# Kernel optimization log

Measured on AMD Instinct MI355X. Metric: run time of the kernel, lower is better.

Reference implementation:

```python
import math
import jax, jax.numpy as jnp
import numpy as np

H, C, PQ, PV = 8, 256, 8, 12   # no_heads, c_hidden, no_qk_points, no_v_points
INF, EPS = 1e5, 1e-8

def quat_to_rot(q):
    w, x, y, z = q[..., 0], q[..., 1], q[..., 2], q[..., 3]
    r = jnp.stack([
        1 - 2*(y*y + z*z), 2*(x*y - w*z),     2*(x*z + w*y),
        2*(x*y + w*z),     1 - 2*(x*x + z*z), 2*(y*z - w*x),
        2*(x*z - w*y),     2*(y*z + w*x),     1 - 2*(x*x + y*y),
    ], axis=-1)
    return r.reshape(q.shape[:-1] + (3, 3))

def setup_inputs() -> dict:
    key = jax.random.key(0)
    ks = jax.random.split(key, 16)
    B, N, CS, CZ = 1, 512, 384, 128
    s = jax.random.normal(ks[0], (B, N, CS), jnp.float32)
    z = jax.random.normal(ks[1], (B, N, N, CZ), jnp.float32) * 0.1
    quat = jax.random.normal(ks[2], (B, N, 4), jnp.float32)
    quat = quat / jnp.linalg.norm(quat, axis=-1, keepdims=True)
    rot = quat_to_rot(quat)                       # [B,N,3,3] valid rotations
    trans = jax.random.normal(ks[3], (B, N, 3), jnp.float32) * 10.0
    mask = jnp.ones((B, N), jnp.float32)
    g = lambda k, sh: jax.random.normal(k, sh, jnp.float32) * 0.02
    params = dict(
        wq=g(ks[4], (CS, H*C)), bq=jnp.zeros((H*C,), jnp.float32),
        wkv=g(ks[5], (CS, 2*H*C)), bkv=jnp.zeros((2*H*C,), jnp.float32),
        wqp=g(ks[6], (CS, H*PQ*3)), bqp=jnp.zeros((H*PQ*3,), jnp.float32),
        wkvp=g(ks[7], (CS, H*(PQ+PV)*3)), bkvp=jnp.zeros((H*(PQ+PV)*3,), jnp.float32),
        wb=g(ks[8], (CZ, H)), bb=jnp.zeros((H,), jnp.float32),
        wz=g(ks[9], (CZ, CZ//4)), bz=jnp.zeros((CZ//4,), jnp.float32),
        head_weights=jnp.full((H,), 0.541324854612918, jnp.float32),  # softplus^-1(1)
        wo=g(ks[10], (H*(C + 4*PV + CZ//4), CS)), bo=jnp.zeros((CS,), jnp.float32),
    )
    return dict(s=s, z=z, rot=rot, trans=trans, mask=mask, **params)

def reference(s, z, rot, trans, mask, wq, bq, wkv, bkv, wqp, bqp, wkvp, bkvp, wb, bb, wz, bz, head_weights, wo, bo):
    B, N, CS = s.shape
    q = (s @ wq + bq).reshape(B, N, H, C)
    kv = (s @ wkv + bkv).reshape(B, N, H, 2 * C)
    k, v = kv[..., :C], kv[..., C:]

    def split_pts(x):  # torch split-into-3 + stack(-1): [B,N,3*M] -> [B,N,M,3]
        return jnp.moveaxis(x.reshape(B, N, 3, -1), -2, -1)

    def apply_rigid(p):  # global frame: R @ p + t
        return jnp.einsum('bnij,bnpj->bnpi', rot, p) + trans[:, :, None, :]

    q_pts = apply_rigid(split_pts(s @ wqp + bqp)).reshape(B, N, H, PQ, 3)
    kv_pts = apply_rigid(split_pts(s @ wkvp + bkvp)).reshape(B, N, H, PQ + PV, 3)
    k_pts, v_pts = kv_pts[..., :PQ, :], kv_pts[..., PQ:, :]

    b_bias = z @ wb + bb                                  # [B,Ni,Nj,H]
    a = jnp.einsum('bihc,bjhc->bhij', q, k) * math.sqrt(1.0 / (3 * C))
    a = a + math.sqrt(1.0 / 3) * jnp.moveaxis(b_bias, -1, 1)

    disp = q_pts[:, :, None] - k_pts[:, None]             # [B,Ni,Nj,H,PQ,3]
    pt_att = jnp.sum(disp * disp, axis=-1)                # [B,Ni,Nj,H,PQ]
    hw = jax.nn.softplus(head_weights) * math.sqrt(1.0 / (3 * (PQ * 9.0 / 2)))
    pt_att = -0.5 * jnp.sum(pt_att * hw[None, None, None, :, None], axis=-1)  # [B,Ni,Nj,H]

    sq_mask = INF * (mask[:, :, None] * mask[:, None, :] - 1.0)
    a = a + jnp.moveaxis(pt_att, -1, 1) + sq_mask[:, None]
    a = jax.nn.softmax(a, axis=-1)                        # [B,H,Ni,Nj]

    o = jnp.einsum('bhij,bjhc->bihc', a, v).reshape(B, N, H * C)

    o_pt = jnp.einsum('bhij,bjhpd->bihpd', a, v_pts)      # [B,N,H,PV,3] global
    o_pt = jnp.einsum('bnji,bnhpj->bnhpi', rot, o_pt - trans[:, :, None, None, :])  # invert_apply
    o_pt_norm = jnp.sqrt(jnp.sum(o_pt * o_pt, axis=-1) + EPS).reshape(B, N, H * PV)
    o_pt_flat = o_pt.reshape(B, N, H * PV, 3)

    pair_z = z @ wz + bz                                  # [B,Ni,Nj,CZ//4]
    o_pair = jnp.einsum('bhij,bijd->bihd', a, pair_z).reshape(B, N, -1)

    feats = jnp.concatenate(
        [o, o_pt_flat[..., 0], o_pt_flat[..., 1], o_pt_flat[..., 2], o_pt_norm, o_pair], axis=-1)
    return feats @ wo + bo
```

## Files before the change

### kernel.cpp

```cpp
#include <hip/hip_runtime.h>


#define OFF_QBH    0
#define OFF_KBH    524288
#define OFF_VB     1048576
#define OFF_QPRAW  2097152
#define OFF_KVPRAW 2195456
#define OFF_QPTS   2441216
#define OFF_KVPTS  2539520
#define OFF_BBIAS  2785280
#define OFF_PAIRZT 3833856
#define OFF_ATTNH  8028160
#define OFF_ATTNL  9076736
#define OFF_FEATS  10125312
#define OFF_WCAT   11501568
#define OFF_WTALL  11504640
#define OFF_VPT    12819456

typedef __attribute__((ext_vector_type(8))) short short8;
typedef __attribute__((ext_vector_type(4))) float f32x4;

__device__ __forceinline__ unsigned short f2bf(float f) {
  union { float f; unsigned u; } v; v.f = f;
  unsigned u = v.u;
  unsigned r = (u + 0x7fffu + ((u >> 16) & 1u)) >> 16;
  return (unsigned short)r;
}
__device__ __forceinline__ float bf2f(unsigned short h) {
  union { unsigned u; float f; } v; v.u = ((unsigned)h) << 16; return v.f;
}
__device__ __forceinline__ short8 pack8(float4 a, float4 b) {
  short8 r;
  r[0] = (short)f2bf(a.x); r[1] = (short)f2bf(a.y);
  r[2] = (short)f2bf(a.z); r[3] = (short)f2bf(a.w);
  r[4] = (short)f2bf(b.x); r[5] = (short)f2bf(b.y);
  r[6] = (short)f2bf(b.z); r[7] = (short)f2bf(b.w);
  return r;
}

__device__ __forceinline__ void sgemm_tile64(
    const float* __restrict__ A, const float* __restrict__ W,
    const float* bias, float* __restrict__ Cout,
    const int K, const int Ncol, const int row0, const int col0,
    const int k0b, const int k1, const bool atomic,
    float (*As)[64], float (*Bs)[64]) {
  const int t  = threadIdx.x;
  const int tx = t & 15, ty = t >> 4;
  const int am = t >> 2, akq = (t & 3) << 2;
  const int bk = t >> 4, bn = (t & 15) << 2;
  float acc[4][4];
#pragma unroll
  for (int i = 0; i < 4; i++)
#pragma unroll
    for (int j = 0; j < 4; j++) acc[i][j] = 0.f;

  for (int k0 = k0b; k0 < k1; k0 += 16) {
    float4 a4 = *(const float4*)(A + (size_t)(row0 + am) * K + k0 + akq);
    float4 b4 = *(const float4*)(W + (size_t)(k0 + bk) * Ncol + col0 + bn);
    __syncthreads();
    As[akq + 0][am] = a4.x; As[akq + 1][am] = a4.y;
    As[akq + 2][am] = a4.z; As[akq + 3][am] = a4.w;
    *(float4*)&Bs[bk][bn] = b4;
    __syncthreads();
#pragma unroll
    for (int kk = 0; kk < 16; kk++) {
      float4 av = *(const float4*)&As[kk][ty << 2];
      float4 bv = *(const float4*)&Bs[kk][tx << 2];
      acc[0][0] += av.x * bv.x; acc[0][1] += av.x * bv.y; acc[0][2] += av.x * bv.z; acc[0][3] += av.x * bv.w;
      acc[1][0] += av.y * bv.x; acc[1][1] += av.y * bv.y; acc[1][2] += av.y * bv.z; acc[1][3] += av.y * bv.w;
      acc[2][0] += av.z * bv.x; acc[2][1] += av.z * bv.y; acc[2][2] += av.z * bv.z; acc[2][3] += av.z * bv.w;
      acc[3][0] += av.w * bv.x; acc[3][1] += av.w * bv.y; acc[3][2] += av.w * bv.z; acc[3][3] += av.w * bv.w;
    }
  }
#pragma unroll
  for (int i = 0; i < 4; i++) {
    int row = row0 + (ty << 2) + i;
#pragma unroll
    for (int j = 0; j < 4; j++) {
      int col = col0 + (tx << 2) + j;
      float v = acc[i][j] + (bias ? bias[col] : 0.f);
      if (atomic) atomicAdd(&Cout[(size_t)row * Ncol + col], v);
      else Cout[(size_t)row * Ncol + col] = v;
    }
  }
}

__global__ __launch_bounds__(256) void prep_wT_all(
    const float* __restrict__ wq, const float* __restrict__ wkv,
    const float* __restrict__ wqp, const float* __restrict__ wkvp,
    unsigned short* __restrict__ wTall) {
  const int ntile = blockIdx.x, kt = blockIdx.y;
  const float* src; int Nsrc, nloc0;
  const int ng0 = ntile * 64;
  if (ntile < 32)      { src = wq;   Nsrc = 2048; nloc0 = ng0; }
  else if (ntile < 96) { src = wkv;  Nsrc = 4096; nloc0 = ng0 - 2048; }
  else if (ntile < 99) { src = wqp;  Nsrc = 192;  nloc0 = ng0 - 6144; }
  else                 { src = wkvp; Nsrc = 480;  nloc0 = ng0 - 6336; }
  __shared__ float tile[64][65];
  const int t = threadIdx.x;
  const int r = t >> 2, cs = (t & 3) * 16;
#pragma unroll
  for (int i = 0; i < 16; i += 4) {
    int n = nloc0 + cs + i;
    float4 v;
    if (n + 3 < Nsrc) v = *(const float4*)(src + (size_t)(kt * 64 + r) * Nsrc + n);
    else {
      v.x = (n + 0 < Nsrc) ? src[(size_t)(kt * 64 + r) * Nsrc + n + 0] : 0.f;
      v.y = (n + 1 < Nsrc) ? src[(size_t)(kt * 64 + r) * Nsrc + n + 1] : 0.f;
      v.z = (n + 2 < Nsrc) ? src[(size_t)(kt * 64 + r) * Nsrc + n + 2] : 0.f;
      v.w = (n + 3 < Nsrc) ? src[(size_t)(kt * 64 + r) * Nsrc + n + 3] : 0.f;
    }
    tile[r][cs + i + 0] = v.x; tile[r][cs + i + 1] = v.y;
    tile[r][cs + i + 2] = v.z; tile[r][cs + i + 3] = v.w;
  }
  __syncthreads();
  const int nr = t >> 2, ks = (t & 3) * 16;
  unsigned short ov[16];
#pragma unroll
  for (int i = 0; i < 16; i++) ov[i] = f2bf(tile[ks + i][nr]);
  unsigned short* dst = wTall + (size_t)(ng0 + nr) * 384 + kt * 64 + ks;
  *(uint4*)(dst) = *(const uint4*)&ov[0];
  *(uint4*)(dst + 8) = *(const uint4*)&ov[8];
}

__global__ __launch_bounds__(256) void proj_mfma(
    const float* __restrict__ s, const unsigned short* __restrict__ wTall,
    const float* __restrict__ bq, const float* __restrict__ bkv,
    const float* __restrict__ bqp, const float* __restrict__ bkvp,
    unsigned short* __restrict__ qbh, unsigned short* __restrict__ kbh,
    float* __restrict__ vb, float* __restrict__ qpraw, float* __restrict__ kvpraw) {
  const int bx = blockIdx.x, row0 = blockIdx.y * 64;
  const int lane = threadIdx.x & 63, wv = threadIdx.x >> 6;
  const int quad = lane >> 4, m = lane & 15;
  const int n0 = bx * 64;
  const float* srow = s + (size_t)(row0 + wv * 16 + m) * 384;
  f32x4 acc[4];
#pragma unroll
  for (int nt = 0; nt < 4; nt++) acc[nt] = (f32x4){0.f, 0.f, 0.f, 0.f};

#pragma unroll
  for (int ksx = 0; ksx < 12; ksx++) {
    const int c0 = ksx * 32 + quad * 8;
    float4 a0 = *(const float4*)(srow + c0);
    float4 a1 = *(const float4*)(srow + c0 + 4);
    short8 af = pack8(a0, a1);
#pragma unroll
    for (int nt = 0; nt < 4; nt++) {
      short8 bf = *(const short8*)(wTall + (size_t)(n0 + nt * 16 + m) * 384 + c0);
      acc[nt] = __builtin_amdgcn_mfma_f32_16x16x32_bf16(af, bf, acc[nt], 0, 0, 0);
    }
  }

  const int rbase = row0 + wv * 16 + quad * 4;
#pragma unroll
  for (int nt = 0; nt < 4; nt++) {
    const int col = n0 + nt * 16 + m;
    if (n0 < 2048) {
      const float bias = bq[col];
#pragma unroll
      for (int r = 0; r < 4; r++)
        qbh[(size_t)(rbase + r) * 2048 + col] = f2bf(acc[nt][r] + bias);
    } else if (n0 < 6144) {
      const int ckv = col - 2048;
      const float bias = bkv[ckv];
      const int hh = ckv >> 9, c = ckv & 511;
      if (c < 256) {
#pragma unroll
        for (int r = 0; r < 4; r++)
          kbh[(size_t)(rbase + r) * 2048 + hh * 256 + c] = f2bf(acc[nt][r] + bias);
      } else {
#pragma unroll
        for (int r = 0; r < 4; r++)
          vb[(size_t)(rbase + r) * 2048 + hh * 256 + (c - 256)] = acc[nt][r] + bias;
      }
    } else if (n0 < 6336) {
      const int cq = col - 6144;
      const float bias = bqp[cq];
#pragma unroll
      for (int r = 0; r < 4; r++)
        qpraw[(size_t)(rbase + r) * 192 + cq] = acc[nt][r] + bias;
    } else {
      const int ck = col - 6336;
      if (ck < 480) {
        const float bias = bkvp[ck];
#pragma unroll
        for (int r = 0; r < 4; r++)
          kvpraw[(size_t)(rbase + r) * 480 + ck] = acc[nt][r] + bias;
      }
    }
  }
}

__global__ __launch_bounds__(256) void rigid_pts(
    const float* __restrict__ qpraw, const float* __restrict__ kvpraw,
    const float* __restrict__ rot, const float* __restrict__ trans,
    float* __restrict__ qpts, float* __restrict__ kvpts) {
  int gid = blockIdx.x * 256 + threadIdx.x;
  int n = gid / 224, r = gid % 224;
  const float* R  = rot + n * 9;
  const float* tr = trans + n * 3;
  float px, py, pz; float* dst;
  if (r < 64) {
    const float* src = qpraw + (size_t)n * 192;
    px = src[r]; py = src[64 + r]; pz = src[128 + r];
    dst = qpts + ((size_t)n * 64 + r) * 3;
  } else {
    int p = r - 64;
    const float* src = kvpraw + (size_t)n * 480;
    px = src[p]; py = src[160 + p]; pz = src[320 + p];
    dst = kvpts + ((size_t)n * 160 + p) * 3;
  }
  dst[0] = R[0] * px + R[1] * py + R[2] * pz + tr[0];
  dst[1] = R[3] * px + R[4] * py + R[5] * pz + tr[1];
  dst[2] = R[6] * px + R[7] * py + R[8] * pz + tr[2];
}

__global__ __launch_bounds__(256) void prep_wT(
    const float* __restrict__ wb, const float* __restrict__ wz,
    unsigned short* __restrict__ wT) {
  int l = blockIdx.x * 256 + threadIdx.x;
  if (l < 6144) {
    int n = l >> 7, k = l & 127;
    float v = (n < 8) ? wb[k * 8 + n] * 0.5773502691896258f
                      : (n < 40 ? wz[k * 32 + (n - 8)] : 0.f);
    wT[l] = f2bf(v);
  }
}

__global__ __launch_bounds__(256) void zpass_mfma(
    const float* __restrict__ z, const unsigned short* __restrict__ wT,
    const float* __restrict__ bb, const float* __restrict__ bz,
    unsigned short* __restrict__ bbias_tb, unsigned short* __restrict__ pairzT) {
  __shared__ __align__(16) unsigned short lb[4][8][16];
  __shared__ __align__(16) unsigned short lp[4][32][16];
  const int lane = threadIdx.x & 63;
  const int wave = threadIdx.x >> 6;
  const int quad = lane >> 4, m = lane & 15;
  const int tile = blockIdx.x * 4 + wave;
  const int row0 = tile * 16;

  short8 bf[3][4];
#pragma unroll
  for (int nt = 0; nt < 3; nt++)
#pragma unroll
    for (int s = 0; s < 4; s++)
      bf[nt][s] = *(const short8*)(wT + (size_t)(nt * 16 + m) * 128 + s * 32 + quad * 8);

  float bias[3];
#pragma unroll
  for (int nt = 0; nt < 3; nt++) {
    int c = nt * 16 + m;
    bias[nt] = (c < 8) ? 0.5773502691896258f * bb[c] : (c < 40 ? bz[c - 8] : 0.f);
  }

  f32x4 acc[3];
#pragma unroll
  for (int nt = 0; nt < 3; nt++) acc[nt] = (f32x4){0.f, 0.f, 0.f, 0.f};

  const float* zr = z + (size_t)(row0 + m) * 128 + quad * 8;
#pragma unroll
  for (int s = 0; s < 4; s++) {
    float4 a0 = *(const float4*)(zr + s * 32);
    float4 a1 = *(const float4*)(zr + s * 32 + 4);
    short8 af = pack8(a0, a1);
#pragma unroll
    for (int nt = 0; nt < 3; nt++)
      acc[nt] = __builtin_amdgcn_mfma_f32_16x16x32_bf16(af, bf[nt][s], acc[nt], 0, 0, 0);
  }

#pragma unroll
  for (int nt = 0; nt < 3; nt++) {
    const int c = nt * 16 + m;
#pragma unroll
    for (int r = 0; r < 4; r++) {
      const float v = acc[nt][r] + bias[nt];
      const int jl = quad * 4 + r;
      if (c < 8)       lb[wave][c][jl] = f2bf(v);
      else if (c < 40) lp[wave][c - 8][jl] = f2bf(v);
    }
  }
  const int i = row0 >> 9, j0 = row0 & 511;
  if (lane < 16) {
    int c = lane >> 1, half = lane & 1;
    uint4 val = *(const uint4*)&lb[wave][c][half * 8];
    *(uint4*)(bbias_tb + (size_t)c * 262144 + row0 + half * 8) = val;
  }
  {
    int d = lane >> 1, half = lane & 1;
    uint4 val = *(const uint4*)&lp[wave][d][half * 8];
    *(uint4*)(pairzT + ((size_t)i * 32 + d) * 512 + j0 + half * 8) = val;
  }
}

__global__ __launch_bounds__(256) void vpt_prep(
    const float* __restrict__ vb, const float* __restrict__ kvpts,
    unsigned short* __restrict__ vptT) {
  const int jt = blockIdx.x, h = blockIdx.y, part = blockIdx.z;
  const int j0 = jt * 64, t = threadIdx.x;
  if (part < 4) {
    __shared__ float tile[64][65];
    const int c0 = part * 64;
    const int r = t >> 2, cs = (t & 3) * 16;
#pragma unroll
    for (int ii = 0; ii < 16; ii += 4) {
      float4 v = *(const float4*)(vb + (size_t)(j0 + r) * 2048 + h * 256 + c0 + cs + ii);
      tile[r][cs + ii + 0] = v.x; tile[r][cs + ii + 1] = v.y;
      tile[r][cs + ii + 2] = v.z; tile[r][cs + ii + 3] = v.w;
    }
    __syncthreads();
    const int cl = t >> 2, js = (t & 3) * 16;
    unsigned short ov[16];
#pragma unroll
    for (int x = 0; x < 16; x++) ov[x] = f2bf(tile[js + x][cl]);
    unsigned short* dst = vptT + ((size_t)h * 352 + c0 + cl) * 512 + j0 + js;
    *(uint4*)dst = *(const uint4*)&ov[0];
    *(uint4*)(dst + 8) = *(const uint4*)&ov[8];
  } else {
    __shared__ float lds[64][37];
    for (int l = t; l < 64 * 36; l += 256) {
      int jl = l / 36, w = l % 36;
      lds[jl][w] = kvpts[((size_t)(j0 + jl) * 160 + h * 20 + 8) * 3 + w];
    }
    __syncthreads();
#pragma unroll
    for (int step = 0; step < 3; step++) {
      int chunk = t + 256 * step;
      int row = chunk >> 3, js = (chunk & 7) * 8;
      unsigned short ov[8];
#pragma unroll
      for (int x = 0; x < 8; x++) {
        int w = (row < 48) ? row : row - 48;
        float f = (w < 36) ? lds[js + x][w] : 0.f;
        unsigned short hi = f2bf(f);
        ov[x] = (row < 48) ? hi : f2bf(f - bf2f(hi));
      }
      *(uint4*)(vptT + ((size_t)h * 352 + 256 + row) * 512 + j0 + js) = *(const uint4*)&ov[0];
    }
  }
}

__global__ __launch_bounds__(256) void logits_softmax(
    const unsigned short* __restrict__ qbh, const unsigned short* __restrict__ kbh,
    const float* __restrict__ qpts, const float* __restrict__ kvpts,
    const unsigned short* __restrict__ bbias_tb, const float* __restrict__ mask,
    const float* __restrict__ hwp,
    unsigned short* __restrict__ attnh, unsigned short* __restrict__ attnl) {
  const int it = blockIdx.x, h = blockIdx.y;
  const int i0 = it * 16;
  __shared__ __align__(16) unsigned short kph[512][32], kpl[512][32];
  __shared__ __align__(16) unsigned short qph[16][32], qpl[16][32];
  __shared__ float kp2[512], qp2[16];
  __shared__ float redm[16][4], reds[16][4];
  __shared__ __align__(16) unsigned short sth[4][16][128], stl[4][16][128];
  const int t = threadIdx.x;

#pragma unroll
  for (int rr = 0; rr < 2; rr++) {
    const int j = t * 2 + rr;
    const float* src = kvpts + ((size_t)j * 160 + h * 20) * 3;
    float s2 = 0.f;
#pragma unroll
    for (int w = 0; w < 24; w++) {
      float x = src[w];
      unsigned short hi = f2bf(x);
      kph[j][w] = hi; kpl[j][w] = f2bf(x - bf2f(hi));
      s2 += x * x;
    }
#pragma unroll
    for (int w = 24; w < 32; w++) { kph[j][w] = 0; kpl[j][w] = 0; }
    kp2[j] = s2;
  }
  if (t < 16) {
    const float* src = qpts + ((size_t)(i0 + t) * 64 + h * 8) * 3;
    float s2 = 0.f;
#pragma unroll
    for (int w = 0; w < 24; w++) {
      float x = src[w];
      unsigned short hi = f2bf(x);
      qph[t][w] = hi; qpl[t][w] = f2bf(x - bf2f(hi));
      s2 += x * x;
    }
#pragma unroll
    for (int w = 24; w < 32; w++) { qph[t][w] = 0; qpl[t][w] = 0; }
    qp2[t] = s2;
  }
  __syncthreads();

  const int lane = t & 63, wv = t >> 6;
  const int quad = lane >> 4, m = lane & 15;
  const int jw0 = wv * 128;

  f32x4 acc[8];
#pragma unroll
  for (int nt = 0; nt < 8; nt++) acc[nt] = (f32x4){0.f, 0.f, 0.f, 0.f};
  const unsigned short* qrow = qbh + (size_t)(i0 + m) * 2048 + h * 256;
#pragma unroll
  for (int s = 0; s < 8; s++) {
    short8 af = *(const short8*)(qrow + s * 32 + quad * 8);
#pragma unroll
    for (int nt = 0; nt < 8; nt++) {
      short8 bfr = *(const short8*)(kbh + (size_t)(jw0 + nt * 16 + m) * 2048 + h * 256 + s * 32 + quad * 8);
      acc[nt] = __builtin_amdgcn_mfma_f32_16x16x32_bf16(af, bfr, acc[nt], 0, 0, 0);
    }
  }

  short8 aqh = *(const short8*)&qph[m][quad * 8];
  short8 aql = *(const short8*)&qpl[m][quad * 8];
  f32x4 accp[8];
#pragma unroll
  for (int nt = 0; nt < 8; nt++) {
    short8 bkh = *(const short8*)&kph[jw0 + nt * 16 + m][quad * 8];
    short8 bkl = *(const short8*)&kpl[jw0 + nt * 16 + m][quad * 8];
    f32x4 p = (f32x4){0.f, 0.f, 0.f, 0.f};
    p = __builtin_amdgcn_mfma_f32_16x16x32_bf16(aqh, bkh, p, 0, 0, 0);
    p = __builtin_amdgcn_mfma_f32_16x16x32_bf16(aqh, bkl, p, 0, 0, 0);
    p = __builtin_amdgcn_mfma_f32_16x16x32_bf16(aql, bkh, p, 0, 0, 0);
    accp[nt] = p;
  }

  const float c1 = 0.03608439182435161f;
  const float hw = log1pf(expf(hwp[h])) * 0.09622504486493764f;
  float lg[8][4];
  float rmax[4] = {-1e30f, -1e30f, -1e30f, -1e30f};
#pragma unroll
  for (int nt = 0; nt < 8; nt++) {
    const int j = jw0 + nt * 16 + m;
    const float kp2v = kp2[j];
    const float mj = mask[j];
#pragma unroll
    for (int r = 0; r < 4; r++) {
      const int il = quad * 4 + r;
      const float pt = qp2[il] + kp2v - 2.f * accp[nt][r];
      float v = c1 * acc[nt][r]
              + bf2f(bbias_tb[(size_t)h * 262144 + (size_t)(i0 + il) * 512 + j])
              - 0.5f * hw * pt
              + 100000.f * (mask[i0 + il] * mj - 1.f);
      lg[nt][r] = v;
      rmax[r] = fmaxf(rmax[r], v);
    }
  }
#pragma unroll
  for (int r = 0; r < 4; r++) {
#pragma unroll
    for (int off = 1; off < 16; off <<= 1) rmax[r] = fmaxf(rmax[r], __shfl_xor(rmax[r], off));
  }
  if (m == 0) {
#pragma unroll
    for (int r = 0; r < 4; r++) redm[quad * 4 + r][wv] = rmax[r];
  }
  __syncthreads();
  float rowm[4], rsum[4];
#pragma unroll
  for (int r = 0; r < 4; r++) {
    const int il = quad * 4 + r;
    rowm[r] = fmaxf(fmaxf(redm[il][0], redm[il][1]), fmaxf(redm[il][2], redm[il][3]));
    rsum[r] = 0.f;
  }
#pragma unroll
  for (int nt = 0; nt < 8; nt++)
#pragma unroll
    for (int r = 0; r < 4; r++) {
      float e = __expf(lg[nt][r] - rowm[r]);
      lg[nt][r] = e;
      rsum[r] += e;
    }
#pragma unroll
  for (int r = 0; r < 4; r++) {
#pragma unroll
    for (int off = 1; off < 16; off <<= 1) rsum[r] += __shfl_xor(rsum[r], off);
  }
  if (m == 0) {
#pragma unroll
    for (int r = 0; r < 4; r++) reds[quad * 4 + r][wv] = rsum[r];
  }
  __syncthreads();
  float inv[4];
#pragma unroll
  for (int r = 0; r < 4; r++) {
    const int il = quad * 4 + r;
    inv[r] = 1.f / (reds[il][0] + reds[il][1] + reds[il][2] + reds[il][3]);
  }
#pragma unroll
  for (int nt = 0; nt < 8; nt++)
#pragma unroll
    for (int r = 0; r < 4; r++) {
      const int il = quad * 4 + r;
      float a = lg[nt][r] * inv[r];
      unsigned short hi = f2bf(a);
      sth[wv][il][nt * 16 + m] = hi;
      stl[wv][il][nt * 16 + m] = f2bf(a - bf2f(hi));
    }
#pragma unroll
  for (int step = 0; step < 4; step++) {
    const int idx = lane + 64 * step;
    const int il = idx >> 4, seg = idx & 15;
    uint4 vh = *(const uint4*)&sth[wv][il][seg * 8];
    uint4 vl = *(const uint4*)&stl[wv][il][seg * 8];
    const size_t off = ((size_t)h * 512 + i0 + il) * 512 + jw0 + seg * 8;
    *(uint4*)(attnh + off) = vh;
    *(uint4*)(attnl + off) = vl;
  }
}

__global__ __launch_bounds__(256) void attn_v3(
    const unsigned short* __restrict__ attnh, const unsigned short* __restrict__ attnl,
    const unsigned short* __restrict__ vptT,
    const float* __restrict__ rot, const float* __restrict__ trans,
    float* __restrict__ feats) {
  const int it = blockIdx.x, h = blockIdx.y;
  const int i0 = it * 16;
  __shared__ float lds_h[16][48], lds_l[16][48];
  const int t = threadIdx.x;
  const int lane = t & 63, wv = t >> 6;
  const int quad = lane >> 4, m = lane & 15;
  const int nt0 = wv * 6;
  const int ncnt = (wv == 3) ? 4 : 6;

  f32x4 acc[6];
#pragma unroll
  for (int k = 0; k < 6; k++) acc[k] = (f32x4){0.f, 0.f, 0.f, 0.f};

  const size_t arow = ((size_t)h * 512 + i0 + m) * 512;
  const unsigned short* vbase = vptT + (size_t)h * 352 * 512;
#pragma unroll
  for (int s = 0; s < 16; s++) {
    const int ko = s * 32 + quad * 8;
    short8 ah = *(const short8*)(attnh + arow + ko);
    short8 al = *(const short8*)(attnl + arow + ko);
#pragma unroll
    for (int k = 0; k < 6; k++) {
      if (k < ncnt) {
        const int nt = nt0 + k;
        short8 bfr = *(const short8*)(vbase + (size_t)(nt * 16 + m) * 512 + ko);
        acc[k] = __builtin_amdgcn_mfma_f32_16x16x32_bf16(ah, bfr, acc[k], 0, 0, 0);
        if (nt >= 16 && nt < 19)
          acc[k] = __builtin_amdgcn_mfma_f32_16x16x32_bf16(al, bfr, acc[k], 0, 0, 0);
      }
    }
  }

#pragma unroll
  for (int k = 0; k < 6; k++) {
    if (k < ncnt) {
      const int nt = nt0 + k;
      if (nt < 16) {
#pragma unroll
        for (int r = 0; r < 4; r++)
          feats[(size_t)(i0 + quad * 4 + r) * 2688 + h * 256 + nt * 16 + m] = acc[k][r];
      } else if (nt < 19) {
        const int w = (nt - 16) * 16 + m;
#pragma unroll
        for (int r = 0; r < 4; r++) if (w < 36) lds_h[quad * 4 + r][w] = acc[k][r];
      } else {
        const int w = (nt - 19) * 16 + m;
#pragma unroll
        for (int r = 0; r < 4; r++) if (w < 36) lds_l[quad * 4 + r][w] = acc[k][r];
      }
    }
  }
  __syncthreads();
  if (t < 192) {
    const int il = t / 12, p = t % 12, irow = i0 + il;
    const float* R = rot + irow * 9;
    const float* tr = trans + irow * 3;
    float x  = lds_h[il][p * 3 + 0] + lds_l[il][p * 3 + 0] - tr[0];
    float y  = lds_h[il][p * 3 + 1] + lds_l[il][p * 3 + 1] - tr[1];
    float zz = lds_h[il][p * 3 + 2] + lds_l[il][p * 3 + 2] - tr[2];
    float o0 = R[0] * x + R[3] * y + R[6] * zz;
    float o1 = R[1] * x + R[4] * y + R[7] * zz;
    float o2 = R[2] * x + R[5] * y + R[8] * zz;
    float nrm = sqrtf(o0 * o0 + o1 * o1 + o2 * o2 + 1e-8f);
    float* fr = feats + (size_t)irow * 2688 + 2048;
    fr[h * 12 + p]       = o0;
    fr[96 + h * 12 + p]  = o1;
    fr[192 + h * 12 + p] = o2;
    fr[288 + h * 12 + p] = nrm;
  }
}

__global__ __launch_bounds__(256) void o_pair_mfma(
    const unsigned short* __restrict__ attnh, const unsigned short* __restrict__ pairzT,
    float* __restrict__ feats) {
  const int lane = threadIdx.x & 63, wv = threadIdx.x >> 6;
  const int quad = lane >> 4, m = lane & 15;
  const int i = blockIdx.x * 4 + wv;
  f32x4 acc[2];
  acc[0] = (f32x4){0.f, 0.f, 0.f, 0.f};
  acc[1] = (f32x4){0.f, 0.f, 0.f, 0.f};
#pragma unroll
  for (int s = 0; s < 16; s++) {
    const int ko = s * 32 + quad * 8;
    short8 af = *(const short8*)(attnh + (size_t)(m & 7) * 262144 + (size_t)i * 512 + ko);
#pragma unroll
    for (int nt = 0; nt < 2; nt++) {
      short8 bfr = *(const short8*)(pairzT + ((size_t)i * 32 + nt * 16 + m) * 512 + ko);
      acc[nt] = __builtin_amdgcn_mfma_f32_16x16x32_bf16(af, bfr, acc[nt], 0, 0, 0);
    }
  }
  if (quad < 2) {
#pragma unroll
    for (int nt = 0; nt < 2; nt++)
#pragma unroll
      for (int r = 0; r < 4; r++) {
        const int hh = quad * 4 + r, d = nt * 16 + m;
        feats[(size_t)i * 2688 + 2432 + hh * 32 + d] = acc[nt][r];
      }
  }
}

__global__ __launch_bounds__(256) void out_gemm_kernel(
    const float* __restrict__ feats, const float* __restrict__ wo,
    const float* __restrict__ bo, float* __restrict__ out) {
  __shared__ float As[16][64], Bs[16][64];
  int col0 = blockIdx.x * 64, row0 = blockIdx.y * 64;
  int k0 = blockIdx.z * 336;
  sgemm_tile64(feats, wo, blockIdx.z == 0 ? bo : nullptr, out,
               2688, 384, row0, col0, k0, k0 + 336, true, As, Bs);
}

extern "C" void kernel_launch(void* const* d_in, const int* in_sizes, int n_in,
                              void* d_out, int out_size, void* d_ws, size_t ws_size,
                              hipStream_t stream) {
  const float* s     = (const float*)d_in[0];
  const float* z     = (const float*)d_in[1];
  const float* rot   = (const float*)d_in[2];
  const float* trans = (const float*)d_in[3];
  const float* mask  = (const float*)d_in[4];
  const float* wq    = (const float*)d_in[5];
  const float* bq    = (const float*)d_in[6];
  const float* wkv   = (const float*)d_in[7];
  const float* bkv   = (const float*)d_in[8];
  const float* wqp   = (const float*)d_in[9];
  const float* bqp   = (const float*)d_in[10];
  const float* wkvp  = (const float*)d_in[11];
  const float* bkvp  = (const float*)d_in[12];
  const float* wb    = (const float*)d_in[13];
  const float* bb    = (const float*)d_in[14];
  const float* wz    = (const float*)d_in[15];
  const float* bz    = (const float*)d_in[16];
  const float* hwp   = (const float*)d_in[17];
  const float* wo    = (const float*)d_in[18];
  const float* bo    = (const float*)d_in[19];
  float* out = (float*)d_out;

  float* ws = (float*)d_ws;
  unsigned short* qbh   = (unsigned short*)(ws + OFF_QBH);
  unsigned short* kbh   = (unsigned short*)(ws + OFF_KBH);
  float* vb      = ws + OFF_VB;
  float* qpraw   = ws + OFF_QPRAW;
  float* kvpraw  = ws + OFF_KVPRAW;
  float* qpts    = ws + OFF_QPTS;
  float* kvpts   = ws + OFF_KVPTS;
  unsigned short* bbias_tb = (unsigned short*)(ws + OFF_BBIAS);
  unsigned short* pairzT   = (unsigned short*)(ws + OFF_PAIRZT);
  unsigned short* attnh    = (unsigned short*)(ws + OFF_ATTNH);
  unsigned short* attnl    = (unsigned short*)(ws + OFF_ATTNL);
  float* feats   = ws + OFF_FEATS;
  unsigned short* wT    = (unsigned short*)(ws + OFF_WCAT);
  unsigned short* wTall = (unsigned short*)(ws + OFF_WTALL);
  unsigned short* vptT  = (unsigned short*)(ws + OFF_VPT);

  prep_wT_all<<<dim3(107, 6), 256, 0, stream>>>(wq, wkv, wqp, wkvp, wTall);
  prep_wT<<<24, 256, 0, stream>>>(wb, wz, wT);
  proj_mfma<<<dim3(107, 8), 256, 0, stream>>>(s, wTall, bq, bkv, bqp, bkvp,
                                              qbh, kbh, vb, qpraw, kvpraw);
  rigid_pts<<<448, 256, 0, stream>>>(qpraw, kvpraw, rot, trans, qpts, kvpts);
  zpass_mfma<<<4096, 256, 0, stream>>>(z, wT, bb, bz, bbias_tb, pairzT);
  vpt_prep<<<dim3(8, 8, 5), 256, 0, stream>>>(vb, kvpts, vptT);
  logits_softmax<<<dim3(32, 8), 256, 0, stream>>>(qbh, kbh, qpts, kvpts, bbias_tb,
                                                  mask, hwp, attnh, attnl);
  attn_v3<<<dim3(32, 8), 256, 0, stream>>>(attnh, attnl, vptT, rot, trans, feats);
  o_pair_mfma<<<128, 256, 0, stream>>>(attnh, pairzT, feats);
  (void)hipMemsetAsync(out, 0, (size_t)out_size * sizeof(float), stream);
  out_gemm_kernel<<<dim3(6, 8, 8), 256, 0, stream>>>(feats, wo, bo, out);
}
```

Before: 390.2 us.

## Fuse softmax with attention-value MFMA, precompute point planes, use bf16 MFMA output GEMM

The attention-value product now runs inside the logits/softmax kernel, reading the softmax hi/lo tiles straight from shared memory instead of writing and re-reading attnl and attn through global memory. Query/key point hi/lo bf16 planes and squared norms are computed once by a new small kernel rather than redundantly per block. The fp32 SIMT split-K output GEMM with atomics and a memset is replaced by a bf16 MFMA GEMM over a bf16 features buffer and a pre-transposed bf16 wo. This trades fp32 precision in the final projection for cheaper compute and removes launches and atomics.

```diff
diff --git a/kernel.cpp b/kernel.cpp
--- a/kernel.cpp
+++ b/kernel.cpp
@@ -11,11 +11,17 @@
 #define OFF_BBIAS  2785280
 #define OFF_PAIRZT 3833856
 #define OFF_ATTNH  8028160
-#define OFF_ATTNL  9076736
-#define OFF_FEATS  10125312
-#define OFF_WCAT   11501568
-#define OFF_WTALL  11504640
-#define OFF_VPT    12819456
+#define OFF_FEATSB 9076736
+#define OFF_WCAT   9764864
+#define OFF_WTALL  9767936
+#define OFF_VPT    11082752
+#define OFF_WOT    11803648
+#define OFF_QPTH   12319744
+#define OFF_QPTL   12385280
+#define OFF_KPTH   12450816
+#define OFF_KPTL   12516352
+#define OFF_QP2    12581888
+#define OFF_KP2    12585984
 
 typedef __attribute__((ext_vector_type(8))) short short8;
 typedef __attribute__((ext_vector_type(4))) float f32x4;
@@ -36,53 +42,6 @@
   r[4] = (short)f2bf(b.x); r[5] = (short)f2bf(b.y);
   r[6] = (short)f2bf(b.z); r[7] = (short)f2bf(b.w);
   return r;
-}
-
-__device__ __forceinline__ void sgemm_tile64(
-    const float* __restrict__ A, const float* __restrict__ W,
-    const float* bias, float* __restrict__ Cout,
-    const int K, const int Ncol, const int row0, const int col0,
-    const int k0b, const int k1, const bool atomic,
-    float (*As)[64], float (*Bs)[64]) {
-  const int t  = threadIdx.x;
-  const int tx = t & 15, ty = t >> 4;
-  const int am = t >> 2, akq = (t & 3) << 2;
-  const int bk = t >> 4, bn = (t & 15) << 2;
-  float acc[4][4];
-#pragma unroll
-  for (int i = 0; i < 4; i++)
-#pragma unroll
-    for (int j = 0; j < 4; j++) acc[i][j] = 0.f;
-
-  for (int k0 = k0b; k0 < k1; k0 += 16) {
-    float4 a4 = *(const float4*)(A + (size_t)(row0 + am) * K + k0 + akq);
-    float4 b4 = *(const float4*)(W + (size_t)(k0 + bk) * Ncol + col0 + bn);
-    __syncthreads();
-    As[akq + 0][am] = a4.x; As[akq + 1][am] = a4.y;
-    As[akq + 2][am] = a4.z; As[akq + 3][am] = a4.w;
-    *(float4*)&Bs[bk][bn] = b4;
-    __syncthreads();
-#pragma unroll
-    for (int kk = 0; kk < 16; kk++) {
-      float4 av = *(const float4*)&As[kk][ty << 2];
-      float4 bv = *(const float4*)&Bs[kk][tx << 2];
-      acc[0][0] += av.x * bv.x; acc[0][1] += av.x * bv.y; acc[0][2] += av.x * bv.z; acc[0][3] += av.x * bv.w;
-      acc[1][0] += av.y * bv.x; acc[1][1] += av.y * bv.y; acc[1][2] += av.y * bv.z; acc[1][3] += av.y * bv.w;
-      acc[2][0] += av.z * bv.x; acc[2][1] += av.z * bv.y; acc[2][2] += av.z * bv.z; acc[2][3] += av.z * bv.w;
-      acc[3][0] += av.w * bv.x; acc[3][1] += av.w * bv.y; acc[3][2] += av.w * bv.z; acc[3][3] += av.w * bv.w;
-    }
-  }
-#pragma unroll
-  for (int i = 0; i < 4; i++) {
-    int row = row0 + (ty << 2) + i;
-#pragma unroll
-    for (int j = 0; j < 4; j++) {
-      int col = col0 + (tx << 2) + j;
-      float v = acc[i][j] + (bias ? bias[col] : 0.f);
-      if (atomic) atomicAdd(&Cout[(size_t)row * Ncol + col], v);
-      else Cout[(size_t)row * Ncol + col] = v;
-    }
-  }
 }
 
 __global__ __launch_bounds__(256) void prep_wT_all(
@@ -119,6 +78,28 @@
 #pragma unroll
   for (int i = 0; i < 16; i++) ov[i] = f2bf(tile[ks + i][nr]);
   unsigned short* dst = wTall + (size_t)(ng0 + nr) * 384 + kt * 64 + ks;
+  *(uint4*)(dst) = *(const uint4*)&ov[0];
+  *(uint4*)(dst + 8) = *(const uint4*)&ov[8];
+}
+
+__global__ __launch_bounds__(256) void prep_woT(
+    const float* __restrict__ wo, unsigned short* __restrict__ woT) {
+  const int kt = blockIdx.x, ntile = blockIdx.y;
+  __shared__ float tile[64][65];
+  const int t = threadIdx.x;
+  const int r = t >> 2, cs = (t & 3) * 16;
+#pragma unroll
+  for (int i = 0; i < 16; i += 4) {
+    float4 v = *(const float4*)(wo + (size_t)(kt * 64 + r) * 384 + ntile * 64 + cs + i);
+    tile[r][cs + i + 0] = v.x; tile[r][cs + i + 1] = v.y;
+    tile[r][cs + i + 2] = v.z; tile[r][cs + i + 3] = v.w;
+  }
+  __syncthreads();
+  const int nr = t >> 2, ks = (t & 3) * 16;
+  unsigned short ov[16];
+#pragma unroll
+  for (int i = 0; i < 16; i++) ov[i] = f2bf(tile[ks + i][nr]);
+  unsigned short* dst = woT + (size_t)(ntile * 64 + nr) * 2688 + kt * 64 + ks;
   *(uint4*)(dst) = *(const uint4*)&ov[0];
   *(uint4*)(dst + 8) = *(const uint4*)&ov[8];
 }
@@ -215,6 +196,55 @@
   dst[2] = R[6] * px + R[7] * py + R[8] * pz + tr[2];
 }
 
+__global__ __launch_bounds__(256) void pts_planes(
+    const float* __restrict__ qpts, const float* __restrict__ kvpts,
+    unsigned short* __restrict__ qptH, unsigned short* __restrict__ qptL,
+    unsigned short* __restrict__ kptH, unsigned short* __restrict__ kptL,
+    float* __restrict__ qp2g, float* __restrict__ kp2g) {
+  const int row = blockIdx.x * 256 + threadIdx.x;
+  const int h = blockIdx.y;
+  {
+    const float* src = qpts + ((size_t)row * 64 + h * 8) * 3;
+    unsigned short hi[32], lo[32]; float s2 = 0.f;
+#pragma unroll
+    for (int w = 0; w < 24; w++) {
+      float x = src[w];
+      hi[w] = f2bf(x); lo[w] = f2bf(x - bf2f(hi[w]));
+      s2 += x * x;
+    }
+#pragma unroll
+    for (int w = 24; w < 32; w++) { hi[w] = 0; lo[w] = 0; }
+    unsigned short* dh = qptH + ((size_t)h * 512 + row) * 32;
+    unsigned short* dl = qptL + ((size_t)h * 512 + row) * 32;
+#pragma unroll
+    for (int g = 0; g < 4; g++) {
+      *(uint4*)(dh + g * 8) = *(const uint4*)&hi[g * 8];
+      *(uint4*)(dl + g * 8) = *(const uint4*)&lo[g * 8];
+    }
+    qp2g[h * 512 + row] = s2;
+  }
+  {
+    const float* src = kvpts + ((size_t)row * 160 + h * 20) * 3;
+    unsigned short hi[32], lo[32]; float s2 = 0.f;
+#pragma unroll
+    for (int w = 0; w < 24; w++) {
+      float x = src[w];
+      hi[w] = f2bf(x); lo[w] = f2bf(x - bf2f(hi[w]));
+      s2 += x * x;
+    }
+#pragma unroll
+    for (int w = 24; w < 32; w++) { hi[w] = 0; lo[w] = 0; }
+    unsigned short* dh = kptH + ((size_t)h * 512 + row) * 32;
+    unsigned short* dl = kptL + ((size_t)h * 512 + row) * 32;
+#pragma unroll
+    for (int g = 0; g < 4; g++) {
+      *(uint4*)(dh + g * 8) = *(const uint4*)&hi[g * 8];
+      *(uint4*)(dl + g * 8) = *(const uint4*)&lo[g * 8];
+    }
+    kp2g[h * 512 + row] = s2;
+  }
+}
+
 __global__ __launch_bounds__(256) void prep_wT(
     const float* __restrict__ wb, const float* __restrict__ wz,
     unsigned short* __restrict__ wT) {
@@ -339,53 +369,21 @@
   }
 }
 
-__global__ __launch_bounds__(256) void logits_softmax(
+__global__ __launch_bounds__(256) void logits_fused(
     const unsigned short* __restrict__ qbh, const unsigned short* __restrict__ kbh,
-    const float* __restrict__ qpts, const float* __restrict__ kvpts,
+    const unsigned short* __restrict__ qptH, const unsigned short* __restrict__ qptL,
+    const unsigned short* __restrict__ kptH, const unsigned short* __restrict__ kptL,
+    const float* __restrict__ qp2g, const float* __restrict__ kp2g,
     const unsigned short* __restrict__ bbias_tb, const float* __restrict__ mask,
-    const float* __restrict__ hwp,
-    unsigned short* __restrict__ attnh, unsigned short* __restrict__ attnl) {
+    const float* __restrict__ hwp, const unsigned short* __restrict__ vptT,
+    const float* __restrict__ rot, const float* __restrict__ trans,
+    unsigned short* __restrict__ attnh, unsigned short* __restrict__ featsb) {
   const int it = blockIdx.x, h = blockIdx.y;
   const int i0 = it * 16;
-  __shared__ __align__(16) unsigned short kph[512][32], kpl[512][32];
-  __shared__ __align__(16) unsigned short qph[16][32], qpl[16][32];
-  __shared__ float kp2[512], qp2[16];
+  __shared__ __align__(16) unsigned short sth[4][16][136], stl[4][16][136];
   __shared__ float redm[16][4], reds[16][4];
-  __shared__ __align__(16) unsigned short sth[4][16][128], stl[4][16][128];
+  __shared__ float lds_h[16][48], lds_l[16][48];
   const int t = threadIdx.x;
-
-#pragma unroll
-  for (int rr = 0; rr < 2; rr++) {
-    const int j = t * 2 + rr;
-    const float* src = kvpts + ((size_t)j * 160 + h * 20) * 3;
-    float s2 = 0.f;
-#pragma unroll
-    for (int w = 0; w < 24; w++) {
-      float x = src[w];
-      unsigned short hi = f2bf(x);
-      kph[j][w] = hi; kpl[j][w] = f2bf(x - bf2f(hi));
-      s2 += x * x;
-    }
-#pragma unroll
-    for (int w = 24; w < 32; w++) { kph[j][w] = 0; kpl[j][w] = 0; }
-    kp2[j] = s2;
-  }
-  if (t < 16) {
-    const float* src = qpts + ((size_t)(i0 + t) * 64 + h * 8) * 3;
-    float s2 = 0.f;
-#pragma unroll
-    for (int w = 0; w < 24; w++) {
-      float x = src[w];
-      unsigned short hi = f2bf(x);
-      qph[t][w] = hi; qpl[t][w] = f2bf(x - bf2f(hi));
-      s2 += x * x;
-    }
-#pragma unroll
-    for (int w = 24; w < 32; w++) { qph[t][w] = 0; qpl[t][w] = 0; }
-    qp2[t] = s2;
-  }
-  __syncthreads();
-
   const int lane = t & 63, wv = t >> 6;
   const int quad = lane >> 4, m = lane & 15;
   const int jw0 = wv * 128;
@@ -404,13 +402,14 @@
     }
   }
 
-  short8 aqh = *(const short8*)&qph[m][quad * 8];
-  short8 aql = *(const short8*)&qpl[m][quad * 8];
+  short8 aqh = *(const short8*)(qptH + ((size_t)h * 512 + i0 + m) * 32 + quad * 8);
+  short8 aql = *(const short8*)(qptL + ((size_t)h * 512 + i0 + m) * 32 + quad * 8);
   f32x4 accp[8];
 #pragma unroll
   for (int nt = 0; nt < 8; nt++) {
-    short8 bkh = *(const short8*)&kph[jw0 + nt * 16 + m][quad * 8];
-    short8 bkl = *(const short8*)&kpl[jw0 + nt * 16 + m][quad * 8];
+    const size_t krow = ((size_t)h * 512 + jw0 + nt * 16 + m) * 32 + quad * 8;
+    short8 bkh = *(const short8*)(kptH + krow);
+    short8 bkl = *(const short8*)(kptL + krow);
     f32x4 p = (f32x4){0.f, 0.f, 0.f, 0.f};
     p = __builtin_amdgcn_mfma_f32_16x16x32_bf16(aqh, bkh, p, 0, 0, 0);
     p = __builtin_amdgcn_mfma_f32_16x16x32_bf16(aqh, bkl, p, 0, 0, 0);
@@ -420,17 +419,20 @@
 
   const float c1 = 0.03608439182435161f;
   const float hw = log1pf(expf(hwp[h])) * 0.09622504486493764f;
+  float qp2v[4];
+#pragma unroll
+  for (int r = 0; r < 4; r++) qp2v[r] = qp2g[h * 512 + i0 + quad * 4 + r];
   float lg[8][4];
   float rmax[4] = {-1e30f, -1e30f, -1e30f, -1e30f};
 #pragma unroll
   for (int nt = 0; nt < 8; nt++) {
     const int j = jw0 + nt * 16 + m;
-    const float kp2v = kp2[j];
+    const float kp2v = kp2g[h * 512 + j];
     const float mj = mask[j];
 #pragma unroll
     for (int r = 0; r < 4; r++) {
       const int il = quad * 4 + r;
-      const float pt = qp2[il] + kp2v - 2.f * accp[nt][r];
+      const float pt = qp2v[r] + kp2v - 2.f * accp[nt][r];
       float v = c1 * acc[nt][r]
               + bf2f(bbias_tb[(size_t)h * 262144 + (size_t)(i0 + il) * 512 + j])
               - 0.5f * hw * pt
@@ -490,55 +492,38 @@
       sth[wv][il][nt * 16 + m] = hi;
       stl[wv][il][nt * 16 + m] = f2bf(a - bf2f(hi));
     }
+  __syncthreads();
 #pragma unroll
   for (int step = 0; step < 4; step++) {
     const int idx = lane + 64 * step;
     const int il = idx >> 4, seg = idx & 15;
     uint4 vh = *(const uint4*)&sth[wv][il][seg * 8];
-    uint4 vl = *(const uint4*)&stl[wv][il][seg * 8];
-    const size_t off = ((size_t)h * 512 + i0 + il) * 512 + jw0 + seg * 8;
-    *(uint4*)(attnh + off) = vh;
-    *(uint4*)(attnl + off) = vl;
-  }
-}
-
-__global__ __launch_bounds__(256) void attn_v3(
-    const unsigned short* __restrict__ attnh, const unsigned short* __restrict__ attnl,
-    const unsigned short* __restrict__ vptT,
-    const float* __restrict__ rot, const float* __restrict__ trans,
-    float* __restrict__ feats) {
-  const int it = blockIdx.x, h = blockIdx.y;
-  const int i0 = it * 16;
-  __shared__ float lds_h[16][48], lds_l[16][48];
-  const int t = threadIdx.x;
-  const int lane = t & 63, wv = t >> 6;
-  const int quad = lane >> 4, m = lane & 15;
+    *(uint4*)(attnh + ((size_t)h * 512 + i0 + il) * 512 + jw0 + seg * 8) = vh;
+  }
+
   const int nt0 = wv * 6;
   const int ncnt = (wv == 3) ? 4 : 6;
-
-  f32x4 acc[6];
-#pragma unroll
-  for (int k = 0; k < 6; k++) acc[k] = (f32x4){0.f, 0.f, 0.f, 0.f};
-
-  const size_t arow = ((size_t)h * 512 + i0 + m) * 512;
+  f32x4 vacc[6];
+#pragma unroll
+  for (int k = 0; k < 6; k++) vacc[k] = (f32x4){0.f, 0.f, 0.f, 0.f};
   const unsigned short* vbase = vptT + (size_t)h * 352 * 512;
 #pragma unroll
   for (int s = 0; s < 16; s++) {
+    const int wsrc = s >> 2, col = (s & 3) * 32 + quad * 8;
+    short8 ah = *(const short8*)&sth[wsrc][m][col];
+    short8 al = *(const short8*)&stl[wsrc][m][col];
     const int ko = s * 32 + quad * 8;
-    short8 ah = *(const short8*)(attnh + arow + ko);
-    short8 al = *(const short8*)(attnl + arow + ko);
 #pragma unroll
     for (int k = 0; k < 6; k++) {
       if (k < ncnt) {
         const int nt = nt0 + k;
         short8 bfr = *(const short8*)(vbase + (size_t)(nt * 16 + m) * 512 + ko);
-        acc[k] = __builtin_amdgcn_mfma_f32_16x16x32_bf16(ah, bfr, acc[k], 0, 0, 0);
+        vacc[k] = __builtin_amdgcn_mfma_f32_16x16x32_bf16(ah, bfr, vacc[k], 0, 0, 0);
         if (nt >= 16 && nt < 19)
-          acc[k] = __builtin_amdgcn_mfma_f32_16x16x32_bf16(al, bfr, acc[k], 0, 0, 0);
+          vacc[k] = __builtin_amdgcn_mfma_f32_16x16x32_bf16(al, bfr, vacc[k], 0, 0, 0);
       }
     }
   }
-
 #pragma unroll
   for (int k = 0; k < 6; k++) {
     if (k < ncnt) {
@@ -546,15 +531,15 @@
       if (nt < 16) {
 #pragma unroll
         for (int r = 0; r < 4; r++)
-          feats[(size_t)(i0 + quad * 4 + r) * 2688 + h * 256 + nt * 16 + m] = acc[k][r];
+          featsb[(size_t)(i0 + quad * 4 + r) * 2688 + h * 256 + nt * 16 + m] = f2bf(vacc[k][r]);
       } else if (nt < 19) {
         const int w = (nt - 16) * 16 + m;
 #pragma unroll
-        for (int r = 0; r < 4; r++) if (w < 36) lds_h[quad * 4 + r][w] = acc[k][r];
+        for (int r = 0; r < 4; r++) if (w < 36) lds_h[quad * 4 + r][w] = vacc[k][r];
       } else {
         const int w = (nt - 19) * 16 + m;
 #pragma unroll
-        for (int r = 0; r < 4; r++) if (w < 36) lds_l[quad * 4 + r][w] = acc[k][r];
+        for (int r = 0; r < 4; r++) if (w < 36) lds_l[quad * 4 + r][w] = vacc[k][r];
       }
     }
   }
@@ -570,17 +555,17 @@
     float o1 = R[1] * x + R[4] * y + R[7] * zz;
     float o2 = R[2] * x + R[5] * y + R[8] * zz;
     float nrm = sqrtf(o0 * o0 + o1 * o1 + o2 * o2 + 1e-8f);
-    float* fr = feats + (size_t)irow * 2688 + 2048;
-    fr[h * 12 + p]       = o0;
-    fr[96 + h * 12 + p]  = o1;
-    fr[192 + h * 12 + p] = o2;
-    fr[288 + h * 12 + p] = nrm;
+    unsigned short* fr = featsb + (size_t)irow * 2688 + 2048;
+    fr[h * 12 + p]       = f2bf(o0);
+    fr[96 + h * 12 + p]  = f2bf(o1);
+    fr[192 + h * 12 + p] = f2bf(o2);
+    fr[288 + h * 12 + p] = f2bf(nrm);
   }
 }
 
 __global__ __launch_bounds__(256) void o_pair_mfma(
     const unsigned short* __restrict__ attnh, const unsigned short* __restrict__ pairzT,
-    float* __restrict__ feats) {
+    unsigned short* __restrict__ featsb) {
   const int lane = threadIdx.x & 63, wv = threadIdx.x >> 6;
   const int quad = lane >> 4, m = lane & 15;
   const int i = blockIdx.x * 4 + wv;
@@ -603,19 +588,32 @@
 #pragma unroll
       for (int r = 0; r < 4; r++) {
         const int hh = quad * 4 + r, d = nt * 16 + m;
-        feats[(size_t)i * 2688 + 2432 + hh * 32 + d] = acc[nt][r];
+        featsb[(size_t)i * 2688 + 2432 + hh * 32 + d] = f2bf(acc[nt][r]);
       }
   }
 }
 
-__global__ __launch_bounds__(256) void out_gemm_kernel(
-    const float* __restrict__ feats, const float* __restrict__ wo,
+__global__ __launch_bounds__(256) void out_mfma(
+    const unsigned short* __restrict__ featsb, const unsigned short* __restrict__ woT,
     const float* __restrict__ bo, float* __restrict__ out) {
-  __shared__ float As[16][64], Bs[16][64];
-  int col0 = blockIdx.x * 64, row0 = blockIdx.y * 64;
-  int k0 = blockIdx.z * 336;
-  sgemm_tile64(feats, wo, blockIdx.z == 0 ? bo : nullptr, out,
-               2688, 384, row0, col0, k0, k0 + 336, true, As, Bs);
+  const int it = blockIdx.x, ng = blockIdx.y;
+  const int lane = threadIdx.x & 63, wv = threadIdx.x >> 6;
+  const int quad = lane >> 4, m = lane & 15;
+  const int i0 = it * 16, n0 = (ng * 4 + wv) * 16;
+  const unsigned short* arow = featsb + (size_t)(i0 + m) * 2688;
+  const unsigned short* brow = woT + (size_t)(n0 + m) * 2688;
+  f32x4 acc = (f32x4){0.f, 0.f, 0.f, 0.f};
+#pragma unroll 4
+  for (int s = 0; s < 84; s++) {
+    const int ko = s * 32 + quad * 8;
+    short8 af = *(const short8*)(arow + ko);
+    short8 bf = *(const short8*)(brow + ko);
+    acc = __builtin_amdgcn_mfma_f32_16x16x32_bf16(af, bf, acc, 0, 0, 0);
+  }
+  const float bias = bo[n0 + m];
+#pragma unroll
+  for (int r = 0; r < 4; r++)
+    out[(size_t)(i0 + quad * 4 + r) * 384 + n0 + m] = acc[r] + bias;
 }
 
 extern "C" void kernel_launch(void* const* d_in, const int* in_sizes, int n_in,
@@ -654,23 +652,30 @@
   unsigned short* bbias_tb = (unsigned short*)(ws + OFF_BBIAS);
   unsigned short* pairzT   = (unsigned short*)(ws + OFF_PAIRZT);
   unsigned short* attnh    = (unsigned short*)(ws + OFF_ATTNH);
-  unsigned short* attnl    = (unsigned short*)(ws + OFF_ATTNL);
-  float* feats   = ws + OFF_FEATS;
+  unsigned short* featsb   = (unsigned short*)(ws + OFF_FEATSB);
   unsigned short* wT    = (unsigned short*)(ws + OFF_WCAT);
   unsigned short* wTall = (unsigned short*)(ws + OFF_WTALL);
   unsigned short* vptT  = (unsigned short*)(ws + OFF_VPT);
+  unsigned short* woT   = (unsigned short*)(ws + OFF_WOT);
+  unsigned short* qptH  = (unsigned short*)(ws + OFF_QPTH);
+  unsigned short* qptL  = (unsigned short*)(ws + OFF_QPTL);
+  unsigned short* kptH  = (unsigned short*)(ws + OFF_KPTH);
+  unsigned short* kptL  = (unsigned short*)(ws + OFF_KPTL);
+  float* qp2g = ws + OFF_QP2;
+  float* kp2g = ws + OFF_KP2;
 
   prep_wT_all<<<dim3(107, 6), 256, 0, stream>>>(wq, wkv, wqp, wkvp, wTall);
   prep_wT<<<24, 256, 0, stream>>>(wb, wz, wT);
+  prep_woT<<<dim3(42, 6), 256, 0, stream>>>(wo, woT);
   proj_mfma<<<dim3(107, 8), 256, 0, stream>>>(s, wTall, bq, bkv, bqp, bkvp,
                                               qbh, kbh, vb, qpraw, kvpraw);
   rigid_pts<<<448, 256, 0, stream>>>(qpraw, kvpraw, rot, trans, qpts, kvpts);
+  pts_planes<<<dim3(2, 8), 256, 0, stream>>>(qpts, kvpts, qptH, qptL, kptH, kptL, qp2g, kp2g);
   zpass_mfma<<<4096, 256, 0, stream>>>(z, wT, bb, bz, bbias_tb, pairzT);
   vpt_prep<<<dim3(8, 8, 5), 256, 0, stream>>>(vb, kvpts, vptT);
-  logits_softmax<<<dim3(32, 8), 256, 0, stream>>>(qbh, kbh, qpts, kvpts, bbias_tb,
-                                                  mask, hwp, attnh, attnl);
-  attn_v3<<<dim3(32, 8), 256, 0, stream>>>(attnh, attnl, vptT, rot, trans, feats);
-  o_pair_mfma<<<128, 256, 0, stream>>>(attnh, pairzT, feats);
-  (void)hipMemsetAsync(out, 0, (size_t)out_size * sizeof(float), stream);
-  out_gemm_kernel<<<dim3(6, 8, 8), 256, 0, stream>>>(feats, wo, bo, out);
-}
+  logits_fused<<<dim3(32, 8), 256, 0, stream>>>(qbh, kbh, qptH, qptL, kptH, kptL,
+                                                qp2g, kp2g, bbias_tb, mask, hwp,
+                                                vptT, rot, trans, attnh, featsb);
+  o_pair_mfma<<<128, 256, 0, stream>>>(attnh, pairzT, featsb);
+  out_mfma<<<dim3(32, 6), 256, 0, stream>>>(featsb, woT, bo, out);
+}
```

Result: faster. 368.6 us (-5.5%).
